# Kernel tuning notes

Hardware: AMD Instinct MI355X
Metric: run time of the kernel (lower is better)

## Reference

```python
import jax, jax.numpy as jnp
import numpy as np

B, T, C, H, N = 4, 1024, 1024, 16, 64
DW, DA, DV, DG = 64, 64, 64, 160  # LoRA ranks derived from C=1024
LNX_EPS = 0.00064


def layer_norm(h, g, b, eps=1e-5):
    m = h.mean(-1, keepdims=True)
    var = ((h - m) ** 2).mean(-1, keepdims=True)
    return (h - m) * jax.lax.rsqrt(var + eps) * g + b


def token_shift(h):
    # nn.ZeroPad2d((0,0,1,-1)): shift right along T, zero at t=0
    return jnp.pad(h, ((0, 0), (1, 0), (0, 0)))[:, :-1]


def wkv7(r, w, k, v, a, b):
    # RWKV-7 generalized recurrence. Inputs [B,T,C]; w is log-space decay.
    def re(t):
        return t.reshape(B, T, H, N).transpose(1, 0, 2, 3)  # -> [T,B,H,N]
    r, w, k, v, a, b = map(re, (r, w, k, v, a, b))
    dec = jnp.exp(-jnp.exp(w))
    S0 = jnp.zeros((B, H, N, N), r.dtype)  # state: [value_dim, key_dim]
    def step(S, ins):
        r_, d_, k_, v_, a_, b_ = ins
        sa = jnp.einsum('bhij,bhj->bhi', S, a_)
        S = S * d_[:, :, None, :] + sa[..., None] * b_[:, :, None, :] + v_[..., None] * k_[:, :, None, :]
        return S, jnp.einsum('bhij,bhj->bhi', S, r_)
    _, out = jax.lax.scan(step, S0, (r, dec, k, v, a, b))
    return out.transpose(1, 0, 2, 3).reshape(B, T, C)


def _forward(x, v_first, ln1_g, ln1_b, ln2_g, ln2_b, x_r, x_w, x_k_mix, x_v_mix, x_a, x_g,
             w0, w1, w2, a0, a1, a2, v0, v1, v2, g1, g2, k_k, k_a, r_k,
             W_r, W_k, W_v, W_o, lnx_g, lnx_b, xk_c, Wk_ff, Wv_ff):
    # ---- RNW_Tmix (original RWKV-7 path, layer_id > 0) ----
    h = layer_norm(x, ln1_g, ln1_b)
    xx = token_shift(h) - h
    xr = h + xx * x_r
    xw = h + xx * x_w
    xk = h + xx * x_k_mix
    xv = h + xx * x_v_mix
    xa = h + xx * x_a
    xg = h + xx * x_g
    r = xr @ W_r.T
    w = -jax.nn.softplus(-(w0 + jnp.tanh(xw @ w1) @ w2)) - 0.5
    k = xk @ W_k.T
    v = xv @ W_v.T
    v = v + (v_first - v) * jax.nn.sigmoid(v0 + (xv @ v1) @ v2)
    a = jax.nn.sigmoid(a0 + (xa @ a1) @ a2)
    g = jax.nn.sigmoid(xg @ g1) @ g2
    kk = (k * k_k).reshape(B, T, H, N)
    kk = kk / jnp.maximum(jnp.linalg.norm(kk, axis=-1, keepdims=True), 1e-12)
    kk = kk.reshape(B, T, C)
    k = k * (1 + (a - 1) * k_a)
    y = wkv7(r, w, k, v, -kk, kk * a)
    # GroupNorm(H groups of N channels), eps=0.00064
    yg = y.reshape(B, T, H, N)
    m = yg.mean(-1, keepdims=True)
    var = ((yg - m) ** 2).mean(-1, keepdims=True)
    y = ((yg - m) * jax.lax.rsqrt(var + LNX_EPS)).reshape(B, T, C) * lnx_g + lnx_b
    r4 = r.reshape(B, T, H, N)
    k4 = k.reshape(B, T, H, N)
    v4 = v.reshape(B, T, H, N)
    y = y + ((r4 * k4 * r_k).sum(-1, keepdims=True) * v4).reshape(B, T, C)
    x = x + (y * g) @ W_o.T
    # ---- RWKV_CMix_x070 ----
    h2 = layer_norm(x, ln2_g, ln2_b)
    hx = token_shift(h2) - h2
    kf = h2 + hx * xk_c
    kf = jnp.square(jax.nn.relu(kf @ Wk_ff.T))
    x = x + kf @ Wv_ff.T
    return x


def setup_inputs() -> dict:
    key = jax.random.key(0)
    ks = jax.random.split(key, 40)
    it = iter(range(40))
    def rn(shape, s=0.02):
        return (jax.random.normal(ks[next(it)], shape) * s).astype(jnp.float32)
    def ru(shape):
        return jax.random.uniform(ks[next(it)], shape).astype(jnp.float32)
    return {
        'x': rn((B, T, C), 1.0),
        'v_first': rn((B, T, C), 1.0),
        'ln1_g': jnp.ones((C,), jnp.float32), 'ln1_b': jnp.zeros((C,), jnp.float32),
        'ln2_g': jnp.ones((C,), jnp.float32), 'ln2_b': jnp.zeros((C,), jnp.float32),
        'x_r': ru((1, 1, C)), 'x_w': ru((1, 1, C)), 'x_k_mix': ru((1, 1, C)),
        'x_v_mix': ru((1, 1, C)), 'x_a': ru((1, 1, C)), 'x_g': ru((1, 1, C)),
        'w0': rn((1, 1, C), 0.5) - 4.0, 'w1': rn((C, DW)), 'w2': rn((DW, C), 0.1),
        'a0': rn((1, 1, C), 0.3), 'a1': rn((C, DA)), 'a2': rn((DA, C), 0.1),
        'v0': rn((1, 1, C), 0.3) + 0.73, 'v1': rn((C, DV)), 'v2': rn((DV, C), 0.1),
        'g1': rn((C, DG)), 'g2': rn((DG, C), 0.1),
        'k_k': rn((1, 1, C), 0.05) + 0.71, 'k_a': rn((1, 1, C), 0.05) + 1.02,
        'r_k': rn((H, N), 0.05) - 0.04,
        'W_r': rn((C, C)), 'W_k': rn((C, C), 0.002), 'W_v': rn((C, C)), 'W_o': rn((C, C)),
        'lnx_g': jnp.ones((C,), jnp.float32), 'lnx_b': jnp.zeros((C,), jnp.float32),
        'xk_c': ru((1, 1, C)),
        'Wk_ff': rn((4 * C, C)), 'Wv_ff': rn((C, 4 * C)),
    }


def reference(x, v_first, ln1_g, ln1_b, ln2_g, ln2_b, x_r, x_w, x_k_mix, x_v_mix, x_a, x_g,
              w0, w1, w2, a0, a1, a2, v0, v1, v2, g1, g2, k_k, k_a, r_k,
              W_r, W_k, W_v, W_o, lnx_g, lnx_b, xk_c, Wk_ff, Wv_ff):
    return _forward(x, v_first, ln1_g, ln1_b, ln2_g, ln2_b, x_r, x_w, x_k_mix, x_v_mix, x_a, x_g,
                    w0, w1, w2, a0, a1, a2, v0, v1, v2, g1, g2, k_k, k_a, r_k,
                    W_r, W_k, W_v, W_o, lnx_g, lnx_b, xk_c, Wk_ff, Wv_ff)
```

## Files before the change

### kernel.cpp

```cpp
#include <hip/hip_runtime.h>
#include <hip/hip_bf16.h>


#define BB 4
#define TT 1024
#define CC 1024
#define HH 16
#define NHEAD 64
#define MTOK 4096
#define FFDIM 4096

using bf16 = __hip_bfloat16;
typedef __attribute__((ext_vector_type(8))) short short8;
typedef __attribute__((ext_vector_type(4))) float f32x4;

__device__ __forceinline__ float b2f(bf16 x) { return __bfloat162float(x); }
__device__ __forceinline__ bf16 f2b(float x) { return __float2bfloat16(x); }
__device__ __forceinline__ float u2f(unsigned short u) {
  return __uint_as_float((unsigned)u << 16);
}
__device__ __forceinline__ float2 cv2(ushort2 u) {
  return make_float2(u2f(u.x), u2f(u.y));
}
__device__ __forceinline__ float ldin(const void* p, size_t i, int m) {
  return m ? b2f(((const bf16*)p)[i]) : ((const float*)p)[i];
}

__device__ __forceinline__ void async16(const void* g, void* l) {
  __builtin_amdgcn_global_load_lds((const __attribute__((address_space(1))) void*)g,
                                   (__attribute__((address_space(3))) void*)l, 16, 0, 0);
}

__device__ __forceinline__ float rowsum16(float x) {
  int t;
  t = __builtin_amdgcn_update_dpp(0, __float_as_int(x), 0x121, 0xF, 0xF, true);
  x += __int_as_float(t);
  t = __builtin_amdgcn_update_dpp(0, __float_as_int(x), 0x122, 0xF, 0xF, true);
  x += __int_as_float(t);
  t = __builtin_amdgcn_update_dpp(0, __float_as_int(x), 0x124, 0xF, 0xF, true);
  x += __int_as_float(t);
  t = __builtin_amdgcn_update_dpp(0, __float_as_int(x), 0x128, 0xF, 0xF, true);
  x += __int_as_float(t);
  return x;
}

__device__ __forceinline__ float rowsum32(float x) {
  x = rowsum16(x);
#if defined(__has_builtin) && __has_builtin(__builtin_amdgcn_permlane16_swap)
  {
    const unsigned xi = __float_as_uint(x);
    const auto pr = __builtin_amdgcn_permlane16_swap(xi, xi, false, false);
    return __uint_as_float(pr[0]) + __uint_as_float(pr[1]);
  }
#else
  x += __int_as_float(__builtin_amdgcn_ds_swizzle(__float_as_int(x), 0x401F));
  return x;
#endif
}

__global__ void probe_kernel(const unsigned int* g, int* flag) {
  if (threadIdx.x == 0 && blockIdx.x == 0) {
    flag[0] = (g[0] == 0x3F800000u) ? 0 : 1;
    flag[1] = 1;
  }
}

__global__ __launch_bounds__(256) void cvt_all(
    const void* wr, const void* wk, const void* wv, const void* wo,
    const void* wkff, const void* wvff, const int* flagp,
    bf16* wrc, bf16* wkc, bf16* wvc, bf16* woc, bf16* wkffc, bf16* wvffc) {
  const int z = blockIdx.z;
  const void* in; bf16* out; int n4;
  const int nCC4 = CC * CC / 4, nFF4 = FFDIM * CC / 4;
  switch (z) {
    case 0: in = wr;   out = wrc;   n4 = nCC4; break;
    case 1: in = wk;   out = wkc;   n4 = nCC4; break;
    case 2: in = wv;   out = wvc;   n4 = nCC4; break;
    case 3: in = wo;   out = woc;   n4 = nCC4; break;
    case 4: in = wkff; out = wkffc; n4 = nFF4; break;
    default: in = wvff; out = wvffc; n4 = nFF4; break;
  }
  const int fl = *flagp;
  const int i4 = blockIdx.x * 256 + threadIdx.x;
  if (i4 >= n4) return;
  const size_t i = (size_t)i4 * 4;
#pragma unroll
  for (int e = 0; e < 4; ++e) out[i + e] = f2b(ldin(in, i + e, fl));
}

__global__ __launch_bounds__(256) void fillmark_kernel(unsigned short* out, int n) {
  const int i = blockIdx.x * 256 + threadIdx.x;
  if (i < n) out[i] = 0x3F80;
}

template<int XM>
__global__ __launch_bounds__(256) void ln_kernel(const void* __restrict__ x,
    const void* __restrict__ g, const void* __restrict__ be, const int* flagp,
    bf16* __restrict__ out, float eps) {
  const int fl = *flagp;
  const int xm = (XM < 0) ? fl : XM;
  const int tid = threadIdx.x;
  const size_t base = (size_t)blockIdx.x * CC + tid * 4;
  float v[4];
#pragma unroll
  for (int e = 0; e < 4; ++e) v[e] = ldin(x, base + e, xm);
  float s  = v[0] + v[1] + v[2] + v[3];
  float ss = v[0]*v[0] + v[1]*v[1] + v[2]*v[2] + v[3]*v[3];
#pragma unroll
  for (int m = 1; m <= 32; m <<= 1) { s += __shfl_xor(s, m); ss += __shfl_xor(ss, m); }
  __shared__ float red[8];
  const int wave = tid >> 6, lane = tid & 63;
  if (lane == 0) { red[wave] = s; red[4 + wave] = ss; }
  __syncthreads();
  s  = red[0] + red[1] + red[2] + red[3];
  ss = red[4] + red[5] + red[6] + red[7];
  const float mean = s * (1.0f / CC);
  const float var  = ss * (1.0f / CC) - mean * mean;
  const float rstd = rsqrtf(var + eps);
#pragma unroll
  for (int e = 0; e < 4; ++e) {
    const int c = tid * 4 + e;
    out[base + e] = f2b((v[e] - mean) * rstd * ldin(g, c, fl) + ldin(be, c, fl));
  }
}

__global__ __launch_bounds__(256) void mix6_kernel(const bf16* __restrict__ h,
    const void* cr, const void* cw, const void* ck,
    const void* cv, const void* ca, const void* cg, const int* flagp,
    bf16* __restrict__ xr, bf16* __restrict__ xw, bf16* __restrict__ xk,
    bf16* __restrict__ xv, bf16* __restrict__ xa, bf16* __restrict__ xg) {
  const int fl = *flagp;
  const size_t idx = (size_t)blockIdx.x * 256 + threadIdx.x;
  const int c = idx & (CC - 1);
  const int t = (idx >> 10) & (TT - 1);
  const float hv = b2f(h[idx]);
  const float xx = (t == 0 ? 0.f : b2f(h[idx - CC])) - hv;
  xr[idx] = f2b(hv + xx * ldin(cr, c, fl));
  xw[idx] = f2b(hv + xx * ldin(cw, c, fl));
  xk[idx] = f2b(hv + xx * ldin(ck, c, fl));
  xv[idx] = f2b(hv + xx * ldin(cv, c, fl));
  xa[idx] = f2b(hv + xx * ldin(ca, c, fl));
  xg[idx] = f2b(hv + xx * ldin(cg, c, fl));
}

__global__ __launch_bounds__(256) void mix1_kernel(const bf16* __restrict__ h,
    const void* cf, const int* flagp, bf16* __restrict__ out) {
  const int fl = *flagp;
  const size_t idx = (size_t)blockIdx.x * 256 + threadIdx.x;
  const int c = idx & (CC - 1);
  const int t = (idx >> 10) & (TT - 1);
  const float hv = b2f(h[idx]);
  const float xx = (t == 0 ? 0.f : b2f(h[idx - CC])) - hv;
  out[idx] = f2b(hv + xx * ldin(cf, c, fl));
}

__global__ __launch_bounds__(256) void transpose_all(
    const void* w1, const void* a1, const void* v1, const void* g1,
    const void* w2, const void* a2, const void* v2, const void* g2,
    const int* flagp,
    bf16* w1t, bf16* a1t, bf16* v1t, bf16* g1t,
    bf16* w2t, bf16* a2t, bf16* v2t, bf16* g2t) {
  const int z = blockIdx.z;
  const void* in; bf16* out; int R, Cc;
  switch (z) {
    case 0: in = w1; out = w1t; R = CC;  Cc = 64;  break;
    case 1: in = a1; out = a1t; R = CC;  Cc = 64;  break;
    case 2: in = v1; out = v1t; R = CC;  Cc = 64;  break;
    case 3: in = g1; out = g1t; R = CC;  Cc = 160; break;
    case 4: in = w2; out = w2t; R = 64;  Cc = CC;  break;
    case 5: in = a2; out = a2t; R = 64;  Cc = CC;  break;
    case 6: in = v2; out = v2t; R = 64;  Cc = CC;  break;
    default: in = g2; out = g2t; R = 160; Cc = CC; break;
  }
  const int fl = *flagp;
  const int idx = blockIdx.x * 256 + threadIdx.x;
  if (idx >= R * Cc) return;
  const int r = idx / Cc, c = idx - r * Cc;
  out[(size_t)c * R + r] = f2b(ldin(in, idx, fl));
}

__device__ __forceinline__ void gemm_core(const bf16* __restrict__ A,
    const bf16* __restrict__ Bm, bf16* __restrict__ Out, int M, int N, int K,
    int mode, short* As, short* Bs) {
  const int tid  = threadIdx.x;
  const int wave = tid >> 6;
  const int lane = tid & 63;
  const int m0 = blockIdx.y * 128;
  const int n0 = blockIdx.x * 128;
  const int wr = (wave >> 1) * 64;
  const int wc = (wave & 1) * 64;
  const int lrow = lane & 15;
  const int lq   = lane >> 4;
  f32x4 acc[4][4];
#pragma unroll
  for (int i = 0; i < 4; ++i)
#pragma unroll
    for (int j = 0; j < 4; ++j) acc[i][j] = (f32x4){0.f, 0.f, 0.f, 0.f};

  for (int k0 = 0; k0 < K; k0 += 32) {
#pragma unroll
    for (int j = 0; j < 2; ++j) {
      const int chunk = j * 256 + tid;
      const int row = chunk >> 2;
      const int c8  = (chunk & 3) * 8;
      const int ldsbase = (j * 256 + wave * 64) * 8;
      const bf16* ga = A + (size_t)(m0 + row) * K + (k0 + c8);
      int br = n0 + row; br = br < N ? br : N - 1;
      const bf16* gb = Bm + (size_t)br * K + (k0 + c8);
      async16(ga, &As[ldsbase]);
      async16(gb, &Bs[ldsbase]);
    }
    __syncthreads();
    short8 af[4], bfr[4];
#pragma unroll
    for (int mi = 0; mi < 4; ++mi)
      af[mi] = *(const short8*)&As[(wr + mi * 16 + lrow) * 32 + lq * 8];
#pragma unroll
    for (int ni = 0; ni < 4; ++ni)
      bfr[ni] = *(const short8*)&Bs[(wc + ni * 16 + lrow) * 32 + lq * 8];
#pragma unroll
    for (int mi = 0; mi < 4; ++mi)
#pragma unroll
      for (int ni = 0; ni < 4; ++ni)
        acc[mi][ni] = __builtin_amdgcn_mfma_f32_16x16x32_bf16(af[mi], bfr[ni], acc[mi][ni], 0, 0, 0);
    __syncthreads();
  }
#pragma unroll
  for (int mi = 0; mi < 4; ++mi) {
#pragma unroll
    for (int ni = 0; ni < 4; ++ni) {
      const int col = n0 + wc + ni * 16 + lrow;
      if (col < N) {
#pragma unroll
        for (int rr = 0; rr < 4; ++rr) {
          const int rowg = m0 + wr + mi * 16 + lq * 4 + rr;
          const size_t oidx = (size_t)rowg * N + col;
          const float val = acc[mi][ni][rr];
          if (mode == 1) { const float t = val > 0.f ? val : 0.f; Out[oidx] = f2b(t * t); }
          else if (mode == 2) Out[oidx] = f2b(val);
          else if (mode == 3) Out[oidx] = f2b(tanhf(val));
          else Out[oidx] = f2b(1.f / (1.f + expf(-val)));
        }
      }
    }
  }
}

template<int MODE>
__global__ __launch_bounds__(256) void gemm_mf(const bf16* __restrict__ A,
    const bf16* __restrict__ Bm, bf16* __restrict__ Out, int M, int N, int K) {
  __shared__ short As[128 * 32];
  __shared__ short Bs[128 * 32];
  gemm_core(A, Bm, Out, M, N, K, MODE, As, Bs);
}

__global__ __launch_bounds__(256) void gemm_lora1(
    const bf16* xw, const bf16* xa, const bf16* xv, const bf16* xg,
    const bf16* w1t, const bf16* a1t, const bf16* v1t, const bf16* g1t,
    bf16* wm, bf16* am, bf16* vm, bf16* gm) {
  __shared__ short As[128 * 32];
  __shared__ short Bs[128 * 32];
  const int z = blockIdx.z;
  const bf16* A; const bf16* B; bf16* O; int N; int mode;
  if (z == 0)      { A = xw; B = w1t; O = wm; N = 64;  mode = 3; }
  else if (z == 1) { A = xa; B = a1t; O = am; N = 64;  mode = 2; }
  else if (z == 2) { A = xv; B = v1t; O = vm; N = 64;  mode = 2; }
  else             { A = xg; B = g1t; O = gm; N = 160; mode = 4; }
  if ((int)blockIdx.x * 128 >= N) return;
  gemm_core(A, B, O, MTOK, N, CC, mode, As, Bs);
}

__global__ __launch_bounds__(256) void gemm_lora2(
    const bf16* wm, const bf16* am, const bf16* vm, const bf16* gm,
    const bf16* w2t, const bf16* a2t, const bf16* v2t, const bf16* g2t,
    bf16* wl, bf16* al, bf16* vl, bf16* gb) {
  __shared__ short As[128 * 32];
  __shared__ short Bs[128 * 32];
  const int z = blockIdx.z;
  const bf16* A; const bf16* B; bf16* O; int K;
  if (z == 0)      { A = wm; B = w2t; O = wl; K = 64;  }
  else if (z == 1) { A = am; B = a2t; O = al; K = 64;  }
  else if (z == 2) { A = vm; B = v2t; O = vl; K = 64;  }
  else             { A = gm; B = g2t; O = gb; K = 160; }
  gemm_core(A, B, O, MTOK, CC, K, 2, As, Bs);
}

template<int MODE>
__global__ __launch_bounds__(256) void gemm_bt(const bf16* __restrict__ A,
    const void* __restrict__ Bm, const int* bmp, bf16* __restrict__ Out,
    int M, int N, int K) {
  const int bm = *bmp;
  __shared__ float As[64][17];
  __shared__ float Bs[64][17];
  const int tid = threadIdx.x;
  const int m0 = blockIdx.y * 64;
  const int n0 = blockIdx.x * 64;
  const int ty = tid >> 4, tx = tid & 15;
  float acc[4][4] = {};
  for (int k0 = 0; k0 < K; k0 += 16) {
    __syncthreads();
#pragma unroll
    for (int e = 0; e < 4; ++e) {
      const int lin = e * 256 + tid;
      const int row = lin >> 4;
      const int kk  = lin & 15;
      As[row][kk] = b2f(A[(size_t)(m0 + row) * K + k0 + kk]);
      int br = n0 + row; br = br < N ? br : N - 1;
      Bs[row][kk] = ldin(Bm, (size_t)br * K + k0 + kk, bm);
    }
    __syncthreads();
#pragma unroll
    for (int k = 0; k < 16; ++k) {
      float a[4], b[4];
#pragma unroll
      for (int i = 0; i < 4; ++i) a[i] = As[ty * 4 + i][k];
#pragma unroll
      for (int j = 0; j < 4; ++j) b[j] = Bs[tx * 4 + j][k];
#pragma unroll
      for (int i = 0; i < 4; ++i)
#pragma unroll
        for (int j = 0; j < 4; ++j) acc[i][j] += a[i] * b[j];
    }
  }
#pragma unroll
  for (int i = 0; i < 4; ++i) {
    const int rowg = m0 + ty * 4 + i;
#pragma unroll
    for (int j = 0; j < 4; ++j) {
      const int col = n0 + tx * 4 + j;
      if (col < N) {
        const size_t oidx = (size_t)rowg * N + col;
        const float val = acc[i][j];
        if (MODE == 1) { const float t = val > 0.f ? val : 0.f; Out[oidx] = f2b(t * t); }
        else if (MODE == 2) Out[oidx] = f2b(val);
        else if (MODE == 3) Out[oidx] = f2b(tanhf(val));
        else Out[oidx] = f2b(1.f / (1.f + expf(-val)));
      }
    }
  }
}

__global__ __launch_bounds__(256) void combine_kernel(
    bf16* kf, bf16* vf, bf16* wl, bf16* al, bf16* vl,
    const void* vfirst, const void* w0, const void* a0, const void* v0,
    const void* kkp, const void* kap, const int* flagp, float* decp) {
  const int fl = *flagp;
  const int tid = threadIdx.x;
  const size_t base = (size_t)blockIdx.x * CC + tid * 4;
  float kkv[4], av4[4];
  float ssq = 0.f;
#pragma unroll
  for (int e = 0; e < 4; ++e) {
    const int c = tid * 4 + e;
    const size_t idx = base + e;
    const float u = ldin(w0, c, fl) + b2f(wl[idx]);
    const float w = (u > 0.f ? -log1pf(expf(-u)) : u - log1pf(expf(u))) - 0.5f;
    wl[idx] = f2b(w);
    if (decp) decp[idx] = __expf(-__expf(w));
    const float a  = 1.f / (1.f + expf(-(ldin(a0, c, fl) + b2f(al[idx]))));
    const float vg = 1.f / (1.f + expf(-(ldin(v0, c, fl) + b2f(vl[idx]))));
    const float v = b2f(vf[idx]);
    vf[idx] = f2b(v + (ldin(vfirst, idx, fl) - v) * vg);
    const float kv = b2f(kf[idx]);
    const float kkr = kv * ldin(kkp, c, fl);
    kkv[e] = kkr; av4[e] = a;
    ssq += kkr * kkr;
    kf[idx] = f2b(kv * (1.f + (a - 1.f) * ldin(kap, c, fl)));
  }
  ssq += __shfl_xor(ssq, 1); ssq += __shfl_xor(ssq, 2);
  ssq += __shfl_xor(ssq, 4); ssq += __shfl_xor(ssq, 8);
  const float inv = 1.f / fmaxf(sqrtf(ssq), 1e-12f);
#pragma unroll
  for (int e = 0; e < 4; ++e) {
    const size_t idx = base + e;
    const float kkn = kkv[e] * inv;
    al[idx] = f2b(-kkn);
    vl[idx] = f2b(kkn * av4[e]);
  }
}


template<int DF>
__device__ __forceinline__ void wkv_stage(const bf16* rp, const void* wp,
    const bf16* kp, const bf16* vp, const bf16* ap, const bf16* bp,
    size_t cb, char* sb, int wave, int lane) {
  const int hb = wave & 1;
  const size_t g2 = cb + (size_t)(hb * 8 + (lane >> 3)) * CC + (lane & 7) * 8;
  if (wave < 2) {
    async16(rp + g2, sb + 0    + hb * 1024);
    async16(kp + g2, sb + 2048 + hb * 1024);
    async16(ap + g2, sb + 4096 + hb * 1024);
  } else {
    async16(bp + g2, sb + 6144 + hb * 1024);
    async16(vp + g2, sb + 8192 + hb * 1024);
  }
  if constexpr (DF) {
    const size_t gd = cb + (size_t)(wave * 4 + (lane >> 4)) * CC + (lane & 15) * 4;
    async16((const float*)wp + gd, sb + 10240 + wave * 1024);
  } else {
    if (wave >= 2) async16((const bf16*)wp + g2, sb + 10240 + hb * 1024);
  }
}

template<int DF>
__device__ __forceinline__ void wkv_load_step(const char* sb, int t, int j0, int i,
    float2& rv, float2& dv, float2& av, float2& bv, float2& vk) {
  const short* sR = (const short*)sb;
  const short* sK = (const short*)(sb + 2048);
  const short* sA = (const short*)(sb + 4096);
  const short* sB = (const short*)(sb + 6144);
  const unsigned short* sV = (const unsigned short*)(sb + 8192);
  rv = cv2(*(const ushort2*)(const void*)(sR + t * 64 + j0));
  const float2 kv = cv2(*(const ushort2*)(const void*)(sK + t * 64 + j0));
  av = cv2(*(const ushort2*)(const void*)(sA + t * 64 + j0));
  bv = cv2(*(const ushort2*)(const void*)(sB + t * 64 + j0));
  const float vi = u2f(sV[t * 64 + i]);
  if constexpr (DF) {
    const float* sD = (const float*)(sb + 10240);
    dv = *(const float2*)(const void*)(sD + t * 64 + j0);
  } else {
    const short* sW = (const short*)(sb + 10240);
    const float2 wv = cv2(*(const ushort2*)(const void*)(sW + t * 64 + j0));
    dv = make_float2(__expf(-__expf(wv.x)), __expf(-__expf(wv.y)));
  }
  vk = make_float2(vi * kv.x, vi * kv.y);
}

template<int DF>
__global__ __launch_bounds__(256) void wkv_scan(
    const bf16* __restrict__ rp, const void* __restrict__ wp,
    const bf16* __restrict__ kp, const bf16* __restrict__ vp,
    const bf16* __restrict__ ap, const bf16* __restrict__ bp,
    bf16* __restrict__ yp) {
  constexpr int BUFB = DF ? 14336 : 12288;
  __shared__ char sbuf[2][BUFB];
  const int blk = blockIdx.x;
  const int q = blk & 7;
  const int h = (blk >> 3) & (HH - 1);
  const int b = blk >> 7;
  const int tid = threadIdx.x;
  const int wave = tid >> 6;
  const int lane = tid & 63;
  const int rl = tid >> 5;
  const int jq = tid & 31;
  const int j0 = jq * 2;
  const int i = q * 8 + rl;
  const size_t bbase = (size_t)b * TT * CC + (size_t)h * NHEAD;

  float2 S = make_float2(0.f, 0.f);

  wkv_stage<DF>(rp, wp, kp, vp, ap, bp, bbase, sbuf[0], wave, lane);
  __syncthreads();

  for (int c = 0; c < TT / 16; ++c) {
    if (c + 1 < TT / 16)
      wkv_stage<DF>(rp, wp, kp, vp, ap, bp, bbase + (size_t)(c + 1) * 16 * CC,
                    sbuf[(c + 1) & 1], wave, lane);
    const char* sb = sbuf[c & 1];
    size_t yb = bbase + (size_t)c * 16 * CC + i;

    float2 rv, dv, av, bv, vk;
    wkv_load_step<DF>(sb, 0, j0, i, rv, dv, av, bv, vk);
#pragma unroll
    for (int s = 0; s < 16; ++s) {
      float2 rv2, dv2, av2, bv2, vk2;
      if (s + 1 < 16)
        wkv_load_step<DF>(sb, s + 1, j0, i, rv2, dv2, av2, bv2, vk2);
      const float p = fmaf(S.y, av.y, S.x * av.x);
      const float sa = rowsum32(p);
      S.x = fmaf(S.x, dv.x, fmaf(sa, bv.x, vk.x));
      S.y = fmaf(S.y, dv.y, fmaf(sa, bv.y, vk.y));
      const float qv = fmaf(S.y, rv.y, S.x * rv.x);
      const float o = rowsum32(qv);
      if (jq == 0) yp[yb] = f2b(o);
      yb += CC;
      if (s + 1 < 16) { rv = rv2; dv = dv2; av = av2; bv = bv2; vk = vk2; }
    }
    __syncthreads();
  }
}

__global__ __launch_bounds__(256) void post_kernel(
    const bf16* __restrict__ y, const bf16* __restrict__ rp, const bf16* __restrict__ kp,
    const bf16* __restrict__ vp, const bf16* __restrict__ gp,
    const void* rk, const void* lnxg, const void* lnxb, const int* flagp,
    bf16* __restrict__ out) {
  const int fl = *flagp;
  const int tid = threadIdx.x;
  const size_t base = (size_t)blockIdx.x * CC + tid * 4;
  float yv[4];
  float s = 0.f, ssq = 0.f, dot = 0.f;
#pragma unroll
  for (int e = 0; e < 4; ++e) {
    const size_t idx = base + e;
    yv[e] = b2f(y[idx]);
    s += yv[e]; ssq += yv[e] * yv[e];
    dot += b2f(rp[idx]) * b2f(kp[idx]) * ldin(rk, tid * 4 + e, fl);
  }
  s   += __shfl_xor(s, 1);   s   += __shfl_xor(s, 2);   s   += __shfl_xor(s, 4);   s   += __shfl_xor(s, 8);
  ssq += __shfl_xor(ssq, 1); ssq += __shfl_xor(ssq, 2); ssq += __shfl_xor(ssq, 4); ssq += __shfl_xor(ssq, 8);
  dot += __shfl_xor(dot, 1); dot += __shfl_xor(dot, 2); dot += __shfl_xor(dot, 4); dot += __shfl_xor(dot, 8);
  const float m = s * (1.f / NHEAD);
  const float var = ssq * (1.f / NHEAD) - m * m;
  const float rs = rsqrtf(var + 0.00064f);
#pragma unroll
  for (int e = 0; e < 4; ++e) {
    const int c = tid * 4 + e;
    const size_t idx = base + e;
    const float yo = (yv[e] - m) * rs * ldin(lnxg, c, fl) + ldin(lnxb, c, fl)
                     + dot * b2f(vp[idx]);
    out[idx] = f2b(yo * b2f(gp[idx]));
  }
}

__global__ __launch_bounds__(256) void addres_kernel(const void* x, const int* flagp,
    const bf16* __restrict__ o, float* __restrict__ out) {
  const int fl = *flagp;
  const size_t idx = (size_t)blockIdx.x * 256 + threadIdx.x;
  out[idx] = ldin(x, idx, fl) + b2f(o[idx]);
}

__global__ __launch_bounds__(256) void final_kernel(const float* __restrict__ x1,
    const bf16* __restrict__ f, const int* flagp, void* out) {
  const int fl = *flagp;
  const size_t idx = (size_t)blockIdx.x * 256 + threadIdx.x;
  const float v = x1[idx] + b2f(f[idx]);
  if (fl) ((bf16*)out)[idx] = f2b(v);
  else    ((float*)out)[idx] = v;
}

extern "C" void kernel_launch(void* const* d_in, const int* in_sizes, int n_in,
                              void* d_out, int out_size, void* d_ws, size_t ws_size,
                              hipStream_t stream) {
  const void* X      = d_in[0];
  const void* VFIRST = d_in[1];
  const void* LN1G = d_in[2];
  const void* LN1B = d_in[3];
  const void* LN2G = d_in[4];
  const void* LN2B = d_in[5];
  const void* XRC = d_in[6];
  const void* XWC = d_in[7];
  const void* XKC = d_in[8];
  const void* XVC = d_in[9];
  const void* XAC = d_in[10];
  const void* XGC = d_in[11];
  const void* W0p = d_in[12];
  const void* W1p = d_in[13];
  const void* W2p = d_in[14];
  const void* A0p = d_in[15];
  const void* A1p = d_in[16];
  const void* A2p = d_in[17];
  const void* V0p = d_in[18];
  const void* V1p = d_in[19];
  const void* V2p = d_in[20];
  const void* G1p = d_in[21];
  const void* G2p = d_in[22];
  const void* KKp = d_in[23];
  const void* KAp = d_in[24];
  const void* RKp = d_in[25];
  const void* WR  = d_in[26];
  const void* WK  = d_in[27];
  const void* WV  = d_in[28];
  const void* WO  = d_in[29];
  const void* LNXG = d_in[30];
  const void* LNXB = d_in[31];
  const void* XKCF = d_in[32];
  const void* WKFF = d_in[33];
  const void* WVFF = d_in[34];

  const size_t BTC  = (size_t)MTOK * CC;
  const size_t SLOT = BTC * 2;
  char* ws = (char*)d_ws;

  size_t off = 8 * SLOT;
  auto alloc = [&](size_t n) { size_t o = off; off += (n + 255) & ~(size_t)255; return o; };
  const size_t oW1T = alloc((size_t)CC * 64 * 2);
  const size_t oA1T = alloc((size_t)CC * 64 * 2);
  const size_t oV1T = alloc((size_t)CC * 64 * 2);
  const size_t oG1T = alloc((size_t)CC * 160 * 2);
  const size_t oW2T = alloc((size_t)CC * 64 * 2);
  const size_t oA2T = alloc((size_t)CC * 64 * 2);
  const size_t oV2T = alloc((size_t)CC * 64 * 2);
  const size_t oG2T = alloc((size_t)CC * 160 * 2);
  const size_t oWM  = alloc((size_t)MTOK * 64 * 2);
  const size_t oAM  = alloc((size_t)MTOK * 64 * 2);
  const size_t oVM  = alloc((size_t)MTOK * 64 * 2);
  const size_t oGM  = alloc((size_t)MTOK * 160 * 2);
  const size_t oFLG = alloc(8);
  const size_t baseNeed = off;
  const size_t oDEC = alloc(BTC * 4);
  const size_t decNeed = off;
  const size_t oWRc   = alloc((size_t)CC * CC * 2);
  const size_t oWKc   = alloc((size_t)CC * CC * 2);
  const size_t oWVc   = alloc((size_t)CC * CC * 2);
  const size_t oWOc   = alloc((size_t)CC * CC * 2);
  const size_t oWKFFc = alloc((size_t)FFDIM * CC * 2);
  const size_t oWVFFc = alloc((size_t)CC * FFDIM * 2);
  const size_t mfmaNeed = off;

  if (baseNeed > ws_size) {
    fillmark_kernel<<<(out_size + 255) / 256, 256, 0, stream>>>(
        (unsigned short*)d_out, out_size);
    return;
  }
  const bool hasdec = (decNeed <= ws_size);
  const bool useMF  = (mfmaNeed <= ws_size);

  int* FLAG = (int*)(ws + oFLG);
  int* ONE  = FLAG + 1;

  bf16* B0 = (bf16*)(ws + 0 * SLOT);
  bf16* B1 = (bf16*)(ws + 1 * SLOT);
  bf16* B2 = (bf16*)(ws + 2 * SLOT);
  bf16* B3 = (bf16*)(ws + 3 * SLOT);
  bf16* B4 = (bf16*)(ws + 4 * SLOT);
  bf16* B5 = (bf16*)(ws + 5 * SLOT);
  bf16* B6 = (bf16*)(ws + 6 * SLOT);
  bf16* B7 = (bf16*)(ws + 7 * SLOT);
  bf16* Hb  = B0;
  bf16* XRb = B1; bf16* XWb = B2; bf16* XKb = B3;
  bf16* XVb = B4; bf16* XAb = B5; bf16* XGb = B6;
  bf16* Rb  = B7;
  bf16* Kg  = B0;
  bf16* Vg  = B1;
  bf16* WLb = B2;
  bf16* ALb = B3;
  bf16* VLb = B4;
  bf16* Gb  = B5;
  bf16* Yb  = B6;
  bf16* YG  = B2;
  bf16* OBb = B0;
  float* X1b = (float*)(ws + 2 * SLOT);
  bf16* H2b  = B1;
  bf16* KFIN = B0;
  bf16* KACT = B4;
  bf16* FFNb = B1;

  bf16* W1T = (bf16*)(ws + oW1T);
  bf16* A1T = (bf16*)(ws + oA1T);
  bf16* V1T = (bf16*)(ws + oV1T);
  bf16* G1T = (bf16*)(ws + oG1T);
  bf16* W2T = (bf16*)(ws + oW2T);
  bf16* A2T = (bf16*)(ws + oA2T);
  bf16* V2T = (bf16*)(ws + oV2T);
  bf16* G2T = (bf16*)(ws + oG2T);
  bf16* WM  = (bf16*)(ws + oWM);
  bf16* AM  = (bf16*)(ws + oAM);
  bf16* VM  = (bf16*)(ws + oVM);
  bf16* GM  = (bf16*)(ws + oGM);
  float* DECb = (float*)(ws + oDEC);
  float* DECarg = hasdec ? DECb : (float*)nullptr;
  bf16* WRc   = (bf16*)(ws + oWRc);
  bf16* WKc   = (bf16*)(ws + oWKc);
  bf16* WVc   = (bf16*)(ws + oWVc);
  bf16* WOc   = (bf16*)(ws + oWOc);
  bf16* WKFFc = (bf16*)(ws + oWKFFc);
  bf16* WVFFc = (bf16*)(ws + oWVFFc);

  const int EW = (int)(BTC / 256);
  const dim3 blk256(256);

  probe_kernel<<<1, 1, 0, stream>>>((const unsigned int*)LN1G, FLAG);

  ln_kernel<-1><<<MTOK, blk256, 0, stream>>>(X, LN1G, LN1B, FLAG, Hb, 1e-5f);
  mix6_kernel<<<EW, blk256, 0, stream>>>(Hb, XRC, XWC, XKC, XVC, XAC, XGC, FLAG,
                                         XRb, XWb, XKb, XVb, XAb, XGb);
  transpose_all<<<dim3(640, 1, 8), blk256, 0, stream>>>(
      W1p, A1p, V1p, G1p, W2p, A2p, V2p, G2p, FLAG,
      W1T, A1T, V1T, G1T, W2T, A2T, V2T, G2T);

  if (useMF) {
    cvt_all<<<dim3(4096, 1, 6), blk256, 0, stream>>>(
        WR, WK, WV, WO, WKFF, WVFF, FLAG, WRc, WKc, WVc, WOc, WKFFc, WVFFc);

    const dim3 gCC(8, 32), gFF1(32, 32);
    gemm_lora1<<<dim3(2, 32, 4), blk256, 0, stream>>>(
        XWb, XAb, XVb, XGb, W1T, A1T, V1T, G1T, WM, AM, VM, GM);
    gemm_mf<2><<<gCC, blk256, 0, stream>>>(XRb, WRc, Rb, MTOK, CC, CC);
    gemm_mf<2><<<gCC, blk256, 0, stream>>>(XKb, WKc, Kg, MTOK, CC, CC);
    gemm_mf<2><<<gCC, blk256, 0, stream>>>(XVb, WVc, Vg, MTOK, CC, CC);
    gemm_lora2<<<dim3(8, 32, 4), blk256, 0, stream>>>(
        WM, AM, VM, GM, W2T, A2T, V2T, G2T, WLb, ALb, VLb, Gb);

    combine_kernel<<<MTOK, blk256, 0, stream>>>(Kg, Vg, WLb, ALb, VLb, VFIRST,
                                                W0p, A0p, V0p, KKp, KAp, FLAG, DECarg);
    if (hasdec)
      wkv_scan<1><<<BB * HH * 8, blk256, 0, stream>>>(Rb, DECb, Kg, Vg, ALb, VLb, Yb);
    else
      wkv_scan<0><<<BB * HH * 8, blk256, 0, stream>>>(Rb, WLb, Kg, Vg, ALb, VLb, Yb);
    post_kernel<<<MTOK, blk256, 0, stream>>>(Yb, Rb, Kg, Vg, Gb, RKp, LNXG, LNXB, FLAG, YG);
    gemm_mf<2><<<gCC, blk256, 0, stream>>>(YG, WOc, OBb, MTOK, CC, CC);
    addres_kernel<<<EW, blk256, 0, stream>>>(X, FLAG, OBb, X1b);

    ln_kernel<0><<<MTOK, blk256, 0, stream>>>(X1b, LN2G, LN2B, FLAG, H2b, 1e-5f);
    mix1_kernel<<<EW, blk256, 0, stream>>>(H2b, XKCF, FLAG, KFIN);
    gemm_mf<1><<<gFF1, blk256, 0, stream>>>(KFIN, WKFFc, KACT, MTOK, FFDIM, CC);
    gemm_mf<2><<<gCC, blk256, 0, stream>>>(KACT, WVFFc, FFNb, MTOK, CC, FFDIM);
    final_kernel<<<EW, blk256, 0, stream>>>(X1b, FFNb, FLAG, d_out);
  } else {
    const dim3 gCC(16, 64), gL1(1, 64), gG1(3, 64), gFF1(64, 64);
    gemm_bt<3><<<gL1, blk256, 0, stream>>>(XWb, W1T, ONE, WM, MTOK, 64, CC);
    gemm_bt<2><<<gL1, blk256, 0, stream>>>(XAb, A1T, ONE, AM, MTOK, 64, CC);
    gemm_bt<2><<<gL1, blk256, 0, stream>>>(XVb, V1T, ONE, VM, MTOK, 64, CC);
    gemm_bt<4><<<gG1, blk256, 0, stream>>>(XGb, G1T, ONE, GM, MTOK, 160, CC);
    gemm_bt<2><<<gCC, blk256, 0, stream>>>(XRb, WR, FLAG, Rb, MTOK, CC, CC);
    gemm_bt<2><<<gCC, blk256, 0, stream>>>(XKb, WK, FLAG, Kg, MTOK, CC, CC);
    gemm_bt<2><<<gCC, blk256, 0, stream>>>(XVb, WV, FLAG, Vg, MTOK, CC, CC);
    gemm_bt<2><<<gCC, blk256, 0, stream>>>(WM, W2T, ONE, WLb, MTOK, CC, 64);
    gemm_bt<2><<<gCC, blk256, 0, stream>>>(AM, A2T, ONE, ALb, MTOK, CC, 64);
    gemm_bt<2><<<gCC, blk256, 0, stream>>>(VM, V2T, ONE, VLb, MTOK, CC, 64);
    gemm_bt<2><<<gCC, blk256, 0, stream>>>(GM, G2T, ONE, Gb, MTOK, CC, 160);

    combine_kernel<<<MTOK, blk256, 0, stream>>>(Kg, Vg, WLb, ALb, VLb, VFIRST,
                                                W0p, A0p, V0p, KKp, KAp, FLAG, DECarg);
    if (hasdec)
      wkv_scan<1><<<BB * HH * 8, blk256, 0, stream>>>(Rb, DECb, Kg, Vg, ALb, VLb, Yb);
    else
      wkv_scan<0><<<BB * HH * 8, blk256, 0, stream>>>(Rb, WLb, Kg, Vg, ALb, VLb, Yb);
    post_kernel<<<MTOK, blk256, 0, stream>>>(Yb, Rb, Kg, Vg, Gb, RKp, LNXG, LNXB, FLAG, YG);
    gemm_bt<2><<<gCC, blk256, 0, stream>>>(YG, WO, FLAG, OBb, MTOK, CC, CC);
    addres_kernel<<<EW, blk256, 0, stream>>>(X, FLAG, OBb, X1b);

    ln_kernel<0><<<MTOK, blk256, 0, stream>>>(X1b, LN2G, LN2B, FLAG, H2b, 1e-5f);
    mix1_kernel<<<EW, blk256, 0, stream>>>(H2b, XKCF, FLAG, KFIN);
    gemm_bt<1><<<gFF1, blk256, 0, stream>>>(KFIN, WKFF, FLAG, KACT, MTOK, FFDIM, CC);
    gemm_bt<2><<<gCC, blk256, 0, stream>>>(KACT, WVFF, FLAG, FFNb, MTOK, CC, FFDIM);
    final_kernel<<<EW, blk256, 0, stream>>>(X1b, FFNb, FLAG, d_out);
  }

  (void)in_sizes; (void)n_in; (void)out_size;
}
```

Before: 867.4 us.

## Give each WKV scan thread two state rows and defer output reductions

The WKV scan kernel now has each 32-lane group own two value rows of the state instead of one, halving the number of blocks per head. The reductions for the two rows are interleaved, and the output dot product for step s is reduced together with the sa reduction of step s+1, so the DPP and permlane chains overlap. Outputs are collected into one lane per step and written in a single store per chunk instead of a masked store every step. This aims to cut reduction latency and redundant LDS loads per state row, but it halves the grid to 256 blocks, which lowers parallelism across the GPU.

```diff
diff --git a/kernel.cpp b/kernel.cpp
--- a/kernel.cpp
+++ b/kernel.cpp
@@ -13,6 +13,7 @@
 using bf16 = __hip_bfloat16;
 typedef __attribute__((ext_vector_type(8))) short short8;
 typedef __attribute__((ext_vector_type(4))) float f32x4;
+typedef __attribute__((ext_vector_type(2))) unsigned int uint2v;
 
 __device__ __forceinline__ float b2f(bf16 x) { return __bfloat162float(x); }
 __device__ __forceinline__ bf16 f2b(float x) { return __float2bfloat16(x); }
@@ -31,31 +32,35 @@
                                    (__attribute__((address_space(3))) void*)l, 16, 0, 0);
 }
 
-__device__ __forceinline__ float rowsum16(float x) {
-  int t;
-  t = __builtin_amdgcn_update_dpp(0, __float_as_int(x), 0x121, 0xF, 0xF, true);
-  x += __int_as_float(t);
-  t = __builtin_amdgcn_update_dpp(0, __float_as_int(x), 0x122, 0xF, 0xF, true);
-  x += __int_as_float(t);
-  t = __builtin_amdgcn_update_dpp(0, __float_as_int(x), 0x124, 0xF, 0xF, true);
-  x += __int_as_float(t);
-  t = __builtin_amdgcn_update_dpp(0, __float_as_int(x), 0x128, 0xF, 0xF, true);
-  x += __int_as_float(t);
-  return x;
-}
-
-__device__ __forceinline__ float rowsum32(float x) {
-  x = rowsum16(x);
+template<int CTL>
+__device__ __forceinline__ float dppadd(float x) {
+  return x + __int_as_float(
+      __builtin_amdgcn_update_dpp(0, __float_as_int(x), CTL, 0xF, 0xF, true));
+}
+
+__device__ __forceinline__ float plsw(float x) {
 #if defined(__has_builtin) && __has_builtin(__builtin_amdgcn_permlane16_swap)
-  {
-    const unsigned xi = __float_as_uint(x);
-    const auto pr = __builtin_amdgcn_permlane16_swap(xi, xi, false, false);
-    return __uint_as_float(pr[0]) + __uint_as_float(pr[1]);
-  }
+  const unsigned xi = __float_as_uint(x);
+  const uint2v pr = __builtin_amdgcn_permlane16_swap(xi, xi, false, false);
+  return __uint_as_float(pr[0]) + __uint_as_float(pr[1]);
 #else
-  x += __int_as_float(__builtin_amdgcn_ds_swizzle(__float_as_int(x), 0x401F));
-  return x;
+  return x + __int_as_float(__builtin_amdgcn_ds_swizzle(__float_as_int(x), 0x401F));
 #endif
+}
+
+__device__ __forceinline__ void redsum32_2(float& a, float& b) {
+  a = dppadd<0x121>(a); b = dppadd<0x121>(b);
+  a = dppadd<0x122>(a); b = dppadd<0x122>(b);
+  a = dppadd<0x124>(a); b = dppadd<0x124>(b);
+  a = dppadd<0x128>(a); b = dppadd<0x128>(b);
+  a = plsw(a); b = plsw(b);
+}
+__device__ __forceinline__ void redsum32_4(float& a, float& b, float& c, float& d) {
+  a = dppadd<0x121>(a); b = dppadd<0x121>(b); c = dppadd<0x121>(c); d = dppadd<0x121>(d);
+  a = dppadd<0x122>(a); b = dppadd<0x122>(b); c = dppadd<0x122>(c); d = dppadd<0x122>(d);
+  a = dppadd<0x124>(a); b = dppadd<0x124>(b); c = dppadd<0x124>(c); d = dppadd<0x124>(d);
+  a = dppadd<0x128>(a); b = dppadd<0x128>(b); c = dppadd<0x128>(c); d = dppadd<0x128>(d);
+  a = plsw(a); b = plsw(b); c = plsw(c); d = plsw(d);
 }
 
 __global__ void probe_kernel(const unsigned int* g, int* flag) {
@@ -403,8 +408,8 @@
 }
 
 template<int DF>
-__device__ __forceinline__ void wkv_load_step(const char* sb, int t, int j0, int i,
-    float2& rv, float2& dv, float2& av, float2& bv, float2& vk) {
+__device__ __forceinline__ void wkv_load_step2(const char* sb, int t, int j0, int i0,
+    float2& rv, float2& dv, float2& av, float2& bv, float2& vk0, float2& vk1) {
   const short* sR = (const short*)sb;
   const short* sK = (const short*)(sb + 2048);
   const short* sA = (const short*)(sb + 4096);
@@ -414,7 +419,8 @@
   const float2 kv = cv2(*(const ushort2*)(const void*)(sK + t * 64 + j0));
   av = cv2(*(const ushort2*)(const void*)(sA + t * 64 + j0));
   bv = cv2(*(const ushort2*)(const void*)(sB + t * 64 + j0));
-  const float vi = u2f(sV[t * 64 + i]);
+  const ushort2 vp = *(const ushort2*)(const void*)(sV + t * 64 + i0);
+  const float vi0 = u2f(vp.x), vi1 = u2f(vp.y);
   if constexpr (DF) {
     const float* sD = (const float*)(sb + 10240);
     dv = *(const float2*)(const void*)(sD + t * 64 + j0);
@@ -423,7 +429,8 @@
     const float2 wv = cv2(*(const ushort2*)(const void*)(sW + t * 64 + j0));
     dv = make_float2(__expf(-__expf(wv.x)), __expf(-__expf(wv.y)));
   }
-  vk = make_float2(vi * kv.x, vi * kv.y);
+  vk0 = make_float2(vi0 * kv.x, vi0 * kv.y);
+  vk1 = make_float2(vi1 * kv.x, vi1 * kv.y);
 }
 
 template<int DF>
@@ -435,19 +442,20 @@
   constexpr int BUFB = DF ? 14336 : 12288;
   __shared__ char sbuf[2][BUFB];
   const int blk = blockIdx.x;
-  const int q = blk & 7;
-  const int h = (blk >> 3) & (HH - 1);
-  const int b = blk >> 7;
+  const int q = blk & 3;
+  const int h = (blk >> 2) & (HH - 1);
+  const int b = blk >> 6;
   const int tid = threadIdx.x;
   const int wave = tid >> 6;
   const int lane = tid & 63;
-  const int rl = tid >> 5;
+  const int g  = tid >> 5;
   const int jq = tid & 31;
   const int j0 = jq * 2;
-  const int i = q * 8 + rl;
+  const int i0 = q * 16 + g * 2;
   const size_t bbase = (size_t)b * TT * CC + (size_t)h * NHEAD;
 
-  float2 S = make_float2(0.f, 0.f);
+  float2 S0 = make_float2(0.f, 0.f);
+  float2 S1 = make_float2(0.f, 0.f);
 
   wkv_stage<DF>(rp, wp, kp, vp, ap, bp, bbase, sbuf[0], wave, lane);
   __syncthreads();
@@ -457,25 +465,39 @@
       wkv_stage<DF>(rp, wp, kp, vp, ap, bp, bbase + (size_t)(c + 1) * 16 * CC,
                     sbuf[(c + 1) & 1], wave, lane);
     const char* sb = sbuf[c & 1];
-    size_t yb = bbase + (size_t)c * 16 * CC + i;
-
-    float2 rv, dv, av, bv, vk;
-    wkv_load_step<DF>(sb, 0, j0, i, rv, dv, av, bv, vk);
+
+    float2 rv, dv, av, bv, vk0, vk1;
+    wkv_load_step2<DF>(sb, 0, j0, i0, rv, dv, av, bv, vk0, vk1);
+    float q0 = 0.f, q1 = 0.f;
+    float ocol = 0.f;
 #pragma unroll
     for (int s = 0; s < 16; ++s) {
-      float2 rv2, dv2, av2, bv2, vk2;
+      float2 rv2, dv2, av2, bv2, vk02, vk12;
       if (s + 1 < 16)
-        wkv_load_step<DF>(sb, s + 1, j0, i, rv2, dv2, av2, bv2, vk2);
-      const float p = fmaf(S.y, av.y, S.x * av.x);
-      const float sa = rowsum32(p);
-      S.x = fmaf(S.x, dv.x, fmaf(sa, bv.x, vk.x));
-      S.y = fmaf(S.y, dv.y, fmaf(sa, bv.y, vk.y));
-      const float qv = fmaf(S.y, rv.y, S.x * rv.x);
-      const float o = rowsum32(qv);
-      if (jq == 0) yp[yb] = f2b(o);
-      yb += CC;
-      if (s + 1 < 16) { rv = rv2; dv = dv2; av = av2; bv = bv2; vk = vk2; }
+        wkv_load_step2<DF>(sb, s + 1, j0, i0, rv2, dv2, av2, bv2, vk02, vk12);
+      float p0 = fmaf(S0.y, av.y, S0.x * av.x);
+      float p1 = fmaf(S1.y, av.y, S1.x * av.x);
+      if (s == 0) {
+        redsum32_2(p0, p1);
+      } else {
+        redsum32_4(p0, p1, q0, q1);
+        ocol = (jq == s - 1) ? q0 : ocol;
+        ocol = (jq == s - 1 + 16) ? q1 : ocol;
+      }
+      S0.x = fmaf(S0.x, dv.x, fmaf(p0, bv.x, vk0.x));
+      S0.y = fmaf(S0.y, dv.y, fmaf(p0, bv.y, vk0.y));
+      S1.x = fmaf(S1.x, dv.x, fmaf(p1, bv.x, vk1.x));
+      S1.y = fmaf(S1.y, dv.y, fmaf(p1, bv.y, vk1.y));
+      q0 = fmaf(S0.y, rv.y, S0.x * rv.x);
+      q1 = fmaf(S1.y, rv.y, S1.x * rv.x);
+      if (s + 1 < 16) {
+        rv = rv2; dv = dv2; av = av2; bv = bv2; vk0 = vk02; vk1 = vk12;
+      }
     }
+    redsum32_2(q0, q1);
+    ocol = (jq == 15) ? q0 : ocol;
+    ocol = (jq == 31) ? q1 : ocol;
+    yp[bbase + (size_t)(c * 16 + (jq & 15)) * CC + (i0 + (jq >> 4))] = f2b(ocol);
     __syncthreads();
   }
 }
@@ -685,9 +707,9 @@
     combine_kernel<<<MTOK, blk256, 0, stream>>>(Kg, Vg, WLb, ALb, VLb, VFIRST,
                                                 W0p, A0p, V0p, KKp, KAp, FLAG, DECarg);
     if (hasdec)
-      wkv_scan<1><<<BB * HH * 8, blk256, 0, stream>>>(Rb, DECb, Kg, Vg, ALb, VLb, Yb);
+      wkv_scan<1><<<BB * HH * 4, blk256, 0, stream>>>(Rb, DECb, Kg, Vg, ALb, VLb, Yb);
     else
-      wkv_scan<0><<<BB * HH * 8, blk256, 0, stream>>>(Rb, WLb, Kg, Vg, ALb, VLb, Yb);
+      wkv_scan<0><<<BB * HH * 4, blk256, 0, stream>>>(Rb, WLb, Kg, Vg, ALb, VLb, Yb);
     post_kernel<<<MTOK, blk256, 0, stream>>>(Yb, Rb, Kg, Vg, Gb, RKp, LNXG, LNXB, FLAG, YG);
     gemm_mf<2><<<gCC, blk256, 0, stream>>>(YG, WOc, OBb, MTOK, CC, CC);
     addres_kernel<<<EW, blk256, 0, stream>>>(X, FLAG, OBb, X1b);
@@ -714,9 +736,9 @@
     combine_kernel<<<MTOK, blk256, 0, stream>>>(Kg, Vg, WLb, ALb, VLb, VFIRST,
                                                 W0p, A0p, V0p, KKp, KAp, FLAG, DECarg);
     if (hasdec)
-      wkv_scan<1><<<BB * HH * 8, blk256, 0, stream>>>(Rb, DECb, Kg, Vg, ALb, VLb, Yb);
+      wkv_scan<1><<<BB * HH * 4, blk256, 0, stream>>>(Rb, DECb, Kg, Vg, ALb, VLb, Yb);
     else
-      wkv_scan<0><<<BB * HH * 8, blk256, 0, stream>>>(Rb, WLb, Kg, Vg, ALb, VLb, Yb);
+      wkv_scan<0><<<BB * HH * 4, blk256, 0, stream>>>(Rb, WLb, Kg, Vg, ALb, VLb, Yb);
     post_kernel<<<MTOK, blk256, 0, stream>>>(Yb, Rb, Kg, Vg, Gb, RKp, LNXG, LNXB, FLAG, YG);
     gemm_bt<2><<<gCC, blk256, 0, stream>>>(YG, WO, FLAG, OBb, MTOK, CC, CC);
     addres_kernel<<<EW, blk256, 0, stream>>>(X, FLAG, OBb, X1b);
```

Measured after the change: 832.6 us. 4.0% less time.
